# Kernel tuning notes

Measured on AMD Instinct MI355X. Metric: run time of the kernel, lower is better.

The kernel has to match this reference:

```python
import jax, jax.numpy as jnp
import numpy as np

TEMPERATURE = 8.0  # sqrt(d_k), d_k = 64


def setup_inputs() -> dict:
    key = jax.random.key(0)
    kq, kk, kv, km, kr = jax.random.split(key, 5)
    B, H, S, Dk, Dv = 2, 8, 1024, 64, 64
    q = jax.random.normal(kq, (B, H, S, Dk), dtype=jnp.float32)
    k = jax.random.normal(kk, (B, H, S, Dk), dtype=jnp.float32)
    v = jax.random.normal(kv, (B, H, S, Dv), dtype=jnp.float32)
    mask = jax.random.randint(km, (B, 1, S, S), 0, 2, dtype=jnp.int32)
    rpr = jax.random.normal(kr, (B, S, S, Dk), dtype=jnp.float32)
    return {"q": q, "k": k, "v": v, "mask": mask, "rpr": rpr}


def reference(q, k, v, mask, rpr):
    # attn1[b,h,i,j] = sum_d (q/T)[b,h,i,d] * k[b,h,j,d]
    qs = q / TEMPERATURE
    attn1 = jnp.einsum("bhid,bhjd->bhij", qs, k)
    # attn2[b,h,i,j] = sum_d (q/T)[b,h,i,d] * rpr[b,i,j,d]
    attn2 = jnp.einsum("bhid,bijd->bhij", qs, rpr)
    attn = attn1 + attn2
    attn = jnp.where(mask == 0, jnp.float32(-1e9), attn)
    attn = jax.nn.softmax(attn, axis=-1)
    # dropout is identity in eval mode
    output = jnp.einsum("bhij,bhjd->bhid", attn, v)
    return (output, attn)
```

## Files before the change

### kernel.cpp

```cpp
#include <hip/hip_runtime.h>

#define TINV 0.125f
constexpr int S = 1024;
constexpr int D = 64;

__global__ __launch_bounds__(256) void k_attn1(const float* __restrict__ q,
                                               const float* __restrict__ k,
                                               float* __restrict__ attn) {
  __shared__ float Qs[128][36];
  __shared__ float Ks[128][36];
  const int z  = blockIdx.z;
  const int i0 = blockIdx.y * 128;
  const int j0 = blockIdx.x * 128;
  const int t  = threadIdx.x;
  const int tx = t & 15;
  const int ty = t >> 4;

  const float4* qsrc = (const float4*)(q + ((size_t)z * S + i0) * D);
  const float4* ksrc = (const float4*)(k + ((size_t)z * S + j0) * D);

  float acc[8][8];
#pragma unroll
  for (int r = 0; r < 8; ++r)
#pragma unroll
    for (int c = 0; c < 8; ++c) acc[r][c] = 0.f;

#pragma unroll
  for (int p = 0; p < 2; ++p) {
    if (p) __syncthreads();
#pragma unroll
    for (int it = 0; it < 4; ++it) {
      int fidx = t + it * 256;
      int row  = fidx >> 3;
      int c8   = fidx & 7;
      float4 qv = qsrc[row * 16 + p * 8 + c8];
      qv.x *= TINV; qv.y *= TINV; qv.z *= TINV; qv.w *= TINV;
      *(float4*)&Qs[row][c8 * 4] = qv;
      *(float4*)&Ks[row][c8 * 4] = ksrc[row * 16 + p * 8 + c8];
    }
    __syncthreads();
#pragma unroll
    for (int dc = 0; dc < 8; ++dc) {
      float4 kf[8];
#pragma unroll
      for (int c = 0; c < 8; ++c) kf[c] = *(const float4*)&Ks[tx + 16 * c][dc * 4];
#pragma unroll
      for (int r = 0; r < 8; ++r) {
        const float4 qf = *(const float4*)&Qs[ty + 16 * r][dc * 4];
#pragma unroll
        for (int c = 0; c < 8; ++c) {
          acc[r][c] += qf.x * kf[c].x + qf.y * kf[c].y + qf.z * kf[c].z + qf.w * kf[c].w;
        }
      }
    }
  }

  float* dst = attn + ((size_t)z * S + i0) * S + j0;
#pragma unroll
  for (int r = 0; r < 8; ++r)
#pragma unroll
    for (int c = 0; c < 8; ++c)
      dst[(size_t)(ty + 16 * r) * S + tx + 16 * c] = acc[r][c];
}

__global__ __launch_bounds__(256) void k_attn2_softmax(const float* __restrict__ q,
                                                       const float* __restrict__ rpr,
                                                       const int* __restrict__ mask,
                                                       float* __restrict__ attn) {
  __shared__ float qsh[8][64];
  __shared__ float logits[8][1024];
  __shared__ float redA[4][8];
  __shared__ float redB[4][8];

  const int i    = blockIdx.x;
  const int b    = blockIdx.y;
  const int t    = threadIdx.x;
  const int lane = t & 63;
  const int wid  = t >> 6;

  if (t < 128) {
    int h  = t >> 4;
    int c4 = t & 15;
    const float4* src = (const float4*)(q + (((size_t)b * 8 + h) * S + i) * D);
    float4 v = src[c4];
    v.x *= TINV; v.y *= TINV; v.z *= TINV; v.w *= TINV;
    *(float4*)&qsh[h][c4 * 4] = v;
  }
  __syncthreads();

  const float4* rsrc   = (const float4*)(rpr + ((size_t)b * S + i) * (size_t)S * D);
  const float*  a1base = attn + ((size_t)b * 8 * S + i) * S;
  const int*    mrow   = mask + ((size_t)b * S + i) * S;

  for (int jt = 0; jt < 4; ++jt) {
    const int j = t + jt * 256;
    const float4* rrow = rsrc + (size_t)j * 16;
    float acc_h[8];
#pragma unroll
    for (int h = 0; h < 8; ++h) acc_h[h] = 0.f;
#pragma unroll
    for (int half = 0; half < 2; ++half) {
      float4 rv[8];
#pragma unroll
      for (int u = 0; u < 8; ++u) rv[u] = rrow[half * 8 + u];
#pragma unroll
      for (int u = 0; u < 8; ++u) {
        const int dc = half * 8 + u;
#pragma unroll
        for (int h = 0; h < 8; ++h) {
          const float4 qv = *(const float4*)&qsh[h][dc * 4];
          acc_h[h] += rv[u].x * qv.x + rv[u].y * qv.y + rv[u].z * qv.z + rv[u].w * qv.w;
        }
      }
    }
    const int m = mrow[j];
#pragma unroll
    for (int h = 0; h < 8; ++h) {
      float val = acc_h[h] + a1base[(size_t)h * S * S + j];
      logits[h][j] = (m == 0) ? -1e9f : val;
    }
  }

  float lg[8][4];
#pragma unroll
  for (int h = 0; h < 8; ++h)
#pragma unroll
    for (int jt = 0; jt < 4; ++jt) lg[h][jt] = logits[h][t + jt * 256];

  float rmax[8];
#pragma unroll
  for (int h = 0; h < 8; ++h) {
    float m = fmaxf(fmaxf(lg[h][0], lg[h][1]), fmaxf(lg[h][2], lg[h][3]));
#pragma unroll
    for (int off = 32; off >= 1; off >>= 1) m = fmaxf(m, __shfl_xor(m, off));
    if (lane == 0) redA[wid][h] = m;
  }
  __syncthreads();
#pragma unroll
  for (int h = 0; h < 8; ++h)
    rmax[h] = fmaxf(fmaxf(redA[0][h], redA[1][h]), fmaxf(redA[2][h], redA[3][h]));

  float rsum[8];
#pragma unroll
  for (int h = 0; h < 8; ++h) {
#pragma unroll
    for (int jt = 0; jt < 4; ++jt) lg[h][jt] = __expf(lg[h][jt] - rmax[h]);
    float s = lg[h][0] + lg[h][1] + lg[h][2] + lg[h][3];
#pragma unroll
    for (int off = 32; off >= 1; off >>= 1) s += __shfl_xor(s, off);
    if (lane == 0) redB[wid][h] = s;
  }
  __syncthreads();
#pragma unroll
  for (int h = 0; h < 8; ++h)
    rsum[h] = redB[0][h] + redB[1][h] + redB[2][h] + redB[3][h];

  float* adst = attn + ((size_t)b * 8 * S + i) * S;
#pragma unroll
  for (int h = 0; h < 8; ++h) {
    const float inv = 1.0f / rsum[h];
#pragma unroll
    for (int jt = 0; jt < 4; ++jt)
      adst[(size_t)h * S * S + t + jt * 256] = lg[h][jt] * inv;
  }
}

__global__ __launch_bounds__(256) void k_pv(const float* __restrict__ attn,
                                            const float* __restrict__ v,
                                            float* __restrict__ out) {
  __shared__ float Ps[64][68];
  __shared__ float Vs[64][68];
  const int bh = blockIdx.y;
  const int i0 = blockIdx.x * 64;
  const int t  = threadIdx.x;
  const int tx = t & 15;
  const int ty = t >> 4;

  float acc[4][4];
#pragma unroll
  for (int r = 0; r < 4; ++r)
#pragma unroll
    for (int c = 0; c < 4; ++c) acc[r][c] = 0.f;

  const float*  abase = attn + ((size_t)bh * S + i0) * S;
  const float4* vbase = (const float4*)(v + (size_t)bh * S * D);

  for (int jt = 0; jt < 16; ++jt) {
    if (jt) __syncthreads();
    const int j0 = jt * 64;
#pragma unroll
    for (int it = 0; it < 4; ++it) {
      int fidx = t + it * 256;
      int row  = fidx >> 4;
      int c4   = fidx & 15;
      *(float4*)&Ps[row][c4 * 4] = *(const float4*)(abase + (size_t)row * S + j0 + c4 * 4);
      *(float4*)&Vs[row][c4 * 4] = vbase[(size_t)(j0 + row) * 16 + c4];
    }
    __syncthreads();
#pragma unroll
    for (int jc = 0; jc < 16; ++jc) {
      float vr[4][4];
#pragma unroll
      for (int jj = 0; jj < 4; ++jj) {
        float4 tv = *(const float4*)&Vs[jc * 4 + jj][tx * 4];
        vr[jj][0] = tv.x; vr[jj][1] = tv.y; vr[jj][2] = tv.z; vr[jj][3] = tv.w;
      }
#pragma unroll
      for (int r = 0; r < 4; ++r) {
        float4 pf = *(const float4*)&Ps[ty + 16 * r][jc * 4];
        float pa[4] = {pf.x, pf.y, pf.z, pf.w};
#pragma unroll
        for (int c = 0; c < 4; ++c) {
#pragma unroll
          for (int jj = 0; jj < 4; ++jj) acc[r][c] += pa[jj] * vr[jj][c];
        }
      }
    }
  }

  float* obase = out + (size_t)bh * S * D;
#pragma unroll
  for (int r = 0; r < 4; ++r) {
    float4 st = make_float4(acc[r][0], acc[r][1], acc[r][2], acc[r][3]);
    *(float4*)(obase + (size_t)(i0 + ty + 16 * r) * D + tx * 4) = st;
  }
}

extern "C" void kernel_launch(void* const* d_in, const int* in_sizes, int n_in,
                              void* d_out, int out_size, void* d_ws, size_t ws_size,
                              hipStream_t stream) {
  const float* q    = (const float*)d_in[0];
  const float* k    = (const float*)d_in[1];
  const float* v    = (const float*)d_in[2];
  const int*   mask = (const int*)d_in[3];
  const float* rpr  = (const float*)d_in[4];

  float* out  = (float*)d_out;
  float* attn = out + (size_t)2 * 8 * S * D;

  hipLaunchKernelGGL(k_attn1,         dim3(8, 8, 16), dim3(256), 0, stream, q, k, attn);
  hipLaunchKernelGGL(k_attn2_softmax, dim3(1024, 2),  dim3(256), 0, stream, q, rpr, mask, attn);
  hipLaunchKernelGGL(k_pv,            dim3(16, 16),   dim3(256), 0, stream, attn, v, out);
}
```

Measured before the change: 1.046 ms.

## Keep logits in registers, use nontemporal loads, split PV tiles with swizzled grid

The softmax kernel now keeps each thread's logits in registers instead of a 32KB shared-memory array, which raises occupancy. Streaming reads of rpr, mask and attn use nontemporal loads so they do not pollute the cache. The PV kernel halves its row tile to 32 rows, doubling the grid to 512 blocks, and swizzles the block index so neighbouring workgroups spread across (b,h). This buys more parallelism at the cost of reloading V tiles twice as often.

```diff
diff --git a/kernel.cpp b/kernel.cpp
--- a/kernel.cpp
+++ b/kernel.cpp
@@ -3,6 +3,8 @@
 #define TINV 0.125f
 constexpr int S = 1024;
 constexpr int D = 64;
+
+typedef float vf4 __attribute__((ext_vector_type(4)));
 
 __global__ __launch_bounds__(256) void k_attn1(const float* __restrict__ q,
                                                const float* __restrict__ k,
@@ -68,7 +70,6 @@
                                                        const int* __restrict__ mask,
                                                        float* __restrict__ attn) {
   __shared__ float qsh[8][64];
-  __shared__ float logits[8][1024];
   __shared__ float redA[4][8];
   __shared__ float redB[4][8];
 
@@ -88,44 +89,42 @@
   }
   __syncthreads();
 
-  const float4* rsrc   = (const float4*)(rpr + ((size_t)b * S + i) * (size_t)S * D);
-  const float*  a1base = attn + ((size_t)b * 8 * S + i) * S;
-  const int*    mrow   = mask + ((size_t)b * S + i) * S;
-
+  const vf4*   rsrc   = (const vf4*)(rpr + ((size_t)b * S + i) * (size_t)S * D);
+  const float* a1base = attn + ((size_t)b * 8 * S + i) * S;
+  const int*   mrow   = mask + ((size_t)b * S + i) * S;
+
+  float lg[8][4];
+#pragma unroll
   for (int jt = 0; jt < 4; ++jt) {
     const int j = t + jt * 256;
-    const float4* rrow = rsrc + (size_t)j * 16;
+    const vf4* rrow = rsrc + (size_t)j * 16;
     float acc_h[8];
 #pragma unroll
     for (int h = 0; h < 8; ++h) acc_h[h] = 0.f;
 #pragma unroll
     for (int half = 0; half < 2; ++half) {
-      float4 rv[8];
-#pragma unroll
-      for (int u = 0; u < 8; ++u) rv[u] = rrow[half * 8 + u];
+      vf4 rv[8];
+#pragma unroll
+      for (int u = 0; u < 8; ++u)
+        rv[u] = __builtin_nontemporal_load(rrow + half * 8 + u);
 #pragma unroll
       for (int u = 0; u < 8; ++u) {
         const int dc = half * 8 + u;
 #pragma unroll
         for (int h = 0; h < 8; ++h) {
-          const float4 qv = *(const float4*)&qsh[h][dc * 4];
+          const vf4 qv = *(const vf4*)&qsh[h][dc * 4];
           acc_h[h] += rv[u].x * qv.x + rv[u].y * qv.y + rv[u].z * qv.z + rv[u].w * qv.w;
         }
       }
     }
-    const int m = mrow[j];
+    const int m = __builtin_nontemporal_load(mrow + j);
 #pragma unroll
     for (int h = 0; h < 8; ++h) {
-      float val = acc_h[h] + a1base[(size_t)h * S * S + j];
-      logits[h][j] = (m == 0) ? -1e9f : val;
-    }
-  }
-
-  float lg[8][4];
-#pragma unroll
-  for (int h = 0; h < 8; ++h)
-#pragma unroll
-    for (int jt = 0; jt < 4; ++jt) lg[h][jt] = logits[h][t + jt * 256];
+      float a1  = __builtin_nontemporal_load(a1base + (size_t)h * S * S + j);
+      float val = acc_h[h] + a1;
+      lg[h][jt] = (m == 0) ? -1e9f : val;
+    }
+  }
 
   float rmax[8];
 #pragma unroll
@@ -168,33 +167,42 @@
 __global__ __launch_bounds__(256) void k_pv(const float* __restrict__ attn,
                                             const float* __restrict__ v,
                                             float* __restrict__ out) {
-  __shared__ float Ps[64][68];
+  __shared__ float Ps[32][68];
   __shared__ float Vs[64][68];
-  const int bh = blockIdx.y;
-  const int i0 = blockIdx.x * 64;
-  const int t  = threadIdx.x;
-  const int tx = t & 15;
-  const int ty = t >> 4;
-
-  float acc[4][4];
-#pragma unroll
-  for (int r = 0; r < 4; ++r)
+  const int wg  = blockIdx.x + (int)gridDim.x * blockIdx.y;
+  const int swz = (wg & 7) * 64 + (wg >> 3);
+  const int bh  = swz >> 5;
+  const int i0  = (swz & 31) * 32;
+  const int t   = threadIdx.x;
+  const int tx  = t & 15;
+  const int ty  = t >> 4;
+
+  float acc[2][4];
+#pragma unroll
+  for (int r = 0; r < 2; ++r)
 #pragma unroll
     for (int c = 0; c < 4; ++c) acc[r][c] = 0.f;
 
-  const float*  abase = attn + ((size_t)bh * S + i0) * S;
-  const float4* vbase = (const float4*)(v + (size_t)bh * S * D);
+  const float* abase = attn + ((size_t)bh * S + i0) * S;
+  const vf4*   vbase = (const vf4*)(v + (size_t)bh * S * D);
 
   for (int jt = 0; jt < 16; ++jt) {
     if (jt) __syncthreads();
     const int j0 = jt * 64;
+#pragma unroll
+    for (int it = 0; it < 2; ++it) {
+      int fidx = t + it * 256;
+      int row  = fidx >> 4;
+      int c4   = fidx & 15;
+      *(vf4*)&Ps[row][c4 * 4] =
+          __builtin_nontemporal_load((const vf4*)(abase + (size_t)row * S + j0 + c4 * 4));
+    }
 #pragma unroll
     for (int it = 0; it < 4; ++it) {
       int fidx = t + it * 256;
       int row  = fidx >> 4;
       int c4   = fidx & 15;
-      *(float4*)&Ps[row][c4 * 4] = *(const float4*)(abase + (size_t)row * S + j0 + c4 * 4);
-      *(float4*)&Vs[row][c4 * 4] = vbase[(size_t)(j0 + row) * 16 + c4];
+      *(vf4*)&Vs[row][c4 * 4] = vbase[(size_t)(j0 + row) * 16 + c4];
     }
     __syncthreads();
 #pragma unroll
@@ -202,12 +210,12 @@
       float vr[4][4];
 #pragma unroll
       for (int jj = 0; jj < 4; ++jj) {
-        float4 tv = *(const float4*)&Vs[jc * 4 + jj][tx * 4];
+        vf4 tv = *(const vf4*)&Vs[jc * 4 + jj][tx * 4];
         vr[jj][0] = tv.x; vr[jj][1] = tv.y; vr[jj][2] = tv.z; vr[jj][3] = tv.w;
       }
 #pragma unroll
-      for (int r = 0; r < 4; ++r) {
-        float4 pf = *(const float4*)&Ps[ty + 16 * r][jc * 4];
+      for (int r = 0; r < 2; ++r) {
+        vf4 pf = *(const vf4*)&Ps[ty + 16 * r][jc * 4];
         float pa[4] = {pf.x, pf.y, pf.z, pf.w};
 #pragma unroll
         for (int c = 0; c < 4; ++c) {
@@ -220,9 +228,9 @@
 
   float* obase = out + (size_t)bh * S * D;
 #pragma unroll
-  for (int r = 0; r < 4; ++r) {
-    float4 st = make_float4(acc[r][0], acc[r][1], acc[r][2], acc[r][3]);
-    *(float4*)(obase + (size_t)(i0 + ty + 16 * r) * D + tx * 4) = st;
+  for (int r = 0; r < 2; ++r) {
+    vf4 st = {acc[r][0], acc[r][1], acc[r][2], acc[r][3]};
+    *(vf4*)(obase + (size_t)(i0 + ty + 16 * r) * D + tx * 4) = st;
   }
 }
 
@@ -240,5 +248,5 @@
 
   hipLaunchKernelGGL(k_attn1,         dim3(8, 8, 16), dim3(256), 0, stream, q, k, attn);
   hipLaunchKernelGGL(k_attn2_softmax, dim3(1024, 2),  dim3(256), 0, stream, q, rpr, mask, attn);
-  hipLaunchKernelGGL(k_pv,            dim3(16, 16),   dim3(256), 0, stream, attn, v, out);
-}
+  hipLaunchKernelGGL(k_pv,            dim3(32, 16),   dim3(256), 0, stream, attn, v, out);
+}
```

New measurement: 1.472 ms. +40.7%, slower.
